# Performance work log

Hardware: AMD Instinct MI355X
Metric: run time of the kernel (lower is better)

## Reference

```python
import jax, jax.numpy as jnp
import numpy as np

N = 100000
E = 3200000
H_MLP = 30   # EdgeMLP hidden dim
H_GCN = 10   # GCNEvaluator hidden dim
D_IN = 6     # node_dim + token_dim


def setup_inputs() -> dict:
    key = jax.random.key(0)
    ks = jax.random.split(key, 24)
    s = 0.1
    inp = {
        "x": jax.random.normal(ks[0], (N, 1), jnp.float32),
        "token": jax.random.normal(ks[1], (N, 5), jnp.float32),
        "edge_attr_gen": jax.random.normal(ks[2], (E, 1), jnp.float32),
        "edge_attr_eval": jax.random.uniform(ks[3], (E, 2), jnp.float32),
        "gumbel": jax.random.gumbel(ks[4], (E, 2), jnp.float32),
        "edge_index": jax.random.randint(ks[5], (2, E), 0, N, jnp.int32),
        # EdgeMLP params: Linear(13,30), Linear(30,30), Linear(30,30), Linear(30,2)
        "W0": jax.random.normal(ks[6], (2 * D_IN + 1, H_MLP), jnp.float32) * s,
        "b0": jnp.zeros((H_MLP,), jnp.float32),
        "W1": jax.random.normal(ks[7], (H_MLP, H_MLP), jnp.float32) * s,
        "b1": jnp.zeros((H_MLP,), jnp.float32),
        "W2": jax.random.normal(ks[8], (H_MLP, H_MLP), jnp.float32) * s,
        "b2": jnp.zeros((H_MLP,), jnp.float32),
        "W3": jax.random.normal(ks[9], (H_MLP, 2), jnp.float32) * s,
        "b3": jnp.zeros((2,), jnp.float32),
        # GCNEvaluator params
        "Wl": jax.random.normal(ks[10], (1, 1), jnp.float32) * s,   # edge_weight_lin
        "bl": jnp.zeros((1,), jnp.float32),
        "Wc": jax.random.normal(ks[11], (D_IN, H_GCN), jnp.float32) * s,  # GCNConv weight
        "bc": jnp.zeros((H_GCN,), jnp.float32),
        "Wo": jax.random.normal(ks[12], (H_GCN, 1), jnp.float32) * s,     # output Linear
        "bo": jnp.zeros((1,), jnp.float32),
    }
    return inp


def reference(x, token, edge_attr_gen, edge_attr_eval, gumbel, edge_index,
              W0, b0, W1, b1, W2, b2, W3, b3, Wl, bl, Wc, bc, Wo, bo):
    src = edge_index[0]
    tgt = edge_index[1]
    x_all = jnp.concatenate([x, token], axis=-1)              # [N, 6]

    # ---- generate_graph: edge gather + concat + MLP ----
    ef = jnp.concatenate([x_all[src], x_all[tgt], edge_attr_gen], axis=-1)  # [E, 13]
    h = jax.nn.relu(ef @ W0 + b0)
    h = jax.nn.relu(h @ W1 + b1)
    h = jax.nn.relu(h @ W2 + b2)
    logits = h @ W3 + b3                                      # [E, 2]

    # gumbel_softmax(tau=1.0, hard=True) with straight-through
    y_soft = jax.nn.softmax(logits + gumbel, axis=-1)
    y_hard = jax.nn.one_hot(jnp.argmax(y_soft, axis=-1), 2, dtype=y_soft.dtype)
    y = y_hard + y_soft - jax.lax.stop_gradient(y_soft)
    edge_value = y[:, 1:2]                                    # [E, 1]

    # ---- evaluate_graph: GCNEvaluator ----
    combined = jnp.concatenate([edge_attr_eval, edge_value], axis=-1)  # [E, 3]
    mask = combined[:, -2] * (1.0 - combined[:, -1])
    ew = jax.nn.sigmoid((combined[:, :1] @ Wl + bl)[:, 0]) * mask      # [E]

    # GCNConv(add_self_loops=True, normalize=True)
    loop = jnp.arange(N, dtype=src.dtype)
    row = jnp.concatenate([src, loop])
    col = jnp.concatenate([tgt, loop])
    w = jnp.concatenate([ew, jnp.ones((N,), ew.dtype)])
    deg = jax.ops.segment_sum(w, col, num_segments=N)
    dis = jnp.where(deg > 0, jax.lax.rsqrt(jnp.where(deg > 0, deg, 1.0)), 0.0)
    norm = dis[row] * w * dis[col]
    xw = x_all @ Wc                                            # [N, 10]
    agg = jax.ops.segment_sum(norm[:, None] * xw[row], col, num_segments=N) + bc
    out = jax.nn.sigmoid(agg @ Wo + bo)                        # [N, 1]
    return out
```

## Files before the change

kernel.cpp:

```cpp
#include <hip/hip_runtime.h>

#define NN 100000
#define NE 3200000
#define HM 30
#define HG 10
#define MAXK 26
#define OVF_CAP 8192

typedef float __attribute__((ext_vector_type(2))) f32x2;

__device__ __forceinline__ f32x2 pkfma(f32x2 a, f32x2 b, f32x2 c) {
#if __has_builtin(__builtin_elementwise_fma)
    return __builtin_elementwise_fma(a, b, c);
#else
    f32x2 r; r.x = fmaf(a.x, b.x, c.x); r.y = fmaf(a.y, b.y, c.y); return r;
#endif
}

__global__ __launch_bounds__(256) void wtrans_kernel(
    const float* __restrict__ W0, const float* __restrict__ W1,
    const float* __restrict__ W2,
    float* __restrict__ W0T, float* __restrict__ W1T, float* __restrict__ W2T)
{
    for (int idx = threadIdx.x; idx < HM * 16; idx += 256) {
        int j = idx >> 4, i = idx & 15;
        W0T[idx] = (i < 13) ? W0[i * HM + j] : 0.f;
    }
    for (int idx = threadIdx.x; idx < HM * 32; idx += 256) {
        int j = idx >> 5, i = idx & 31;
        float v1 = (i < HM) ? W1[i * HM + j] : 0.f;
        float v2 = (i < HM) ? W2[i * HM + j] : 0.f;
        W1T[idx] = v1;
        W2T[idx] = v2;
    }
}

__global__ __launch_bounds__(256) void pack_kernel(
    const float* __restrict__ x, const float* __restrict__ token,
    const float* __restrict__ Wc,
    float* __restrict__ xall8, float* __restrict__ xwp)
{
    __shared__ float sWc[6 * HG];
    if (threadIdx.x < 6 * HG) sWc[threadIdx.x] = Wc[threadIdx.x];
    __syncthreads();

    int n = blockIdx.x * 256 + threadIdx.x;
    if (n >= NN) return;

    float xa[6];
    xa[0] = x[n];
    #pragma unroll
    for (int i = 0; i < 5; i++) xa[1 + i] = token[n * 5 + i];

    float4* x4 = (float4*)xall8;
    x4[n * 2 + 0] = make_float4(xa[0], xa[1], xa[2], xa[3]);
    x4[n * 2 + 1] = make_float4(xa[4], xa[5], 0.f, 0.f);

    float w[12];
    #pragma unroll
    for (int k = 0; k < HG; k++) {
        float a = 0.f;
        #pragma unroll
        for (int i = 0; i < 6; i++) a = fmaf(xa[i], sWc[i * HG + k], a);
        w[k] = a;
    }
    w[10] = 0.f; w[11] = 0.f;
    float4* wp = (float4*)(xwp + (size_t)n * 12);
    wp[0] = make_float4(w[0], w[1], w[2], w[3]);
    wp[1] = make_float4(w[4], w[5], w[6], w[7]);
    wp[2] = make_float4(w[8], w[9], w[10], w[11]);
}

__global__ __launch_bounds__(256, 2) void edge_mlp6_kernel(
    const float* __restrict__ xall8,
    const float* __restrict__ eg, const float* __restrict__ ee,
    const float* __restrict__ gum, const int* __restrict__ eidx,
    const float* __restrict__ W0T, const float* __restrict__ b0,
    const float* __restrict__ W1T, const float* __restrict__ b1,
    const float* __restrict__ W2T, const float* __restrict__ b2,
    const float* __restrict__ W3, const float* __restrict__ b3,
    const float* __restrict__ Wl, const float* __restrict__ bl,
    float2* __restrict__ slots, int* __restrict__ cnt, float* __restrict__ deg,
    int* __restrict__ ohead, int* __restrict__ onxt,
    float* __restrict__ ovf_w, int* __restrict__ ovf_s, int* __restrict__ novf)
{
    int e = blockIdx.x * 256 + threadIdx.x;
    int s = eidx[e];
    int t = eidx[NE + e];

    const float4* x4 = (const float4*)xall8;
    float4 qa = x4[s * 2], qb = x4[s * 2 + 1];
    float4 qc = x4[t * 2], qd = x4[t * 2 + 1];

    f32x2 ef2[7];
    ef2[0] = f32x2{ qa.x, qa.y };
    ef2[1] = f32x2{ qa.z, qa.w };
    ef2[2] = f32x2{ qb.x, qb.y };
    ef2[3] = f32x2{ qc.x, qc.y };
    ef2[4] = f32x2{ qc.z, qc.w };
    ef2[5] = f32x2{ qd.x, qd.y };
    ef2[6] = f32x2{ eg[e], 0.f };

    float h[HM], g[HM];

    #pragma unroll
    for (int j = 0; j < HM; j++) {
        const f32x2* w2 = (const f32x2*)(W0T + j * 16);
        f32x2 a2 = f32x2{ b0[j], 0.f };
        #pragma unroll
        for (int p = 0; p < 7; p++) a2 = pkfma(ef2[p], w2[p], a2);
        h[j] = fmaxf(a2.x + a2.y, 0.f);
    }

    {
        f32x2 hp[15];
        #pragma unroll
        for (int p = 0; p < 15; p++) hp[p] = f32x2{ h[2 * p], h[2 * p + 1] };
        #pragma unroll
        for (int j = 0; j < HM; j++) {
            const f32x2* w2 = (const f32x2*)(W1T + j * 32);
            f32x2 a2 = f32x2{ b1[j], 0.f };
            #pragma unroll
            for (int p = 0; p < 15; p++) a2 = pkfma(hp[p], w2[p], a2);
            g[j] = fmaxf(a2.x + a2.y, 0.f);
        }
    }
    {
        f32x2 gp[15];
        #pragma unroll
        for (int p = 0; p < 15; p++) gp[p] = f32x2{ g[2 * p], g[2 * p + 1] };
        #pragma unroll
        for (int j = 0; j < HM; j++) {
            const f32x2* w2 = (const f32x2*)(W2T + j * 32);
            f32x2 a2 = f32x2{ b2[j], 0.f };
            #pragma unroll
            for (int p = 0; p < 15; p++) a2 = pkfma(gp[p], w2[p], a2);
            h[j] = fmaxf(a2.x + a2.y, 0.f);
        }
    }

    float l0 = b3[0], l1 = b3[1];
    #pragma unroll
    for (int i = 0; i < HM; i++) {
        l0 = fmaf(h[i], W3[i * 2 + 0], l0);
        l1 = fmaf(h[i], W3[i * 2 + 1], l1);
    }

    const float2 g2 = ((const float2*)gum)[e];
    float v0 = l0 + g2.x;
    float v1 = l1 + g2.y;

    float ew = 0.f;
    if (!(v1 > v0)) {
        const float2 e2 = ((const float2*)ee)[e];
        float z = fmaf(e2.x, Wl[0], bl[0]);
        ew = e2.y / (1.f + __expf(-z));
    }
    if (ew != 0.f) {
        atomicAdd(&deg[t], ew);
        int slot = atomicAdd(&cnt[t], 1);
        if (slot < MAXK) {
            slots[(size_t)t * MAXK + slot] = make_float2(ew, __int_as_float(s));
        } else {
            int i = atomicAdd(novf, 1);
            if (i < OVF_CAP) {
                ovf_w[i] = ew;
                ovf_s[i] = s;
                onxt[i] = atomicExch(&ohead[t], i);
            }
        }
    }
}

__global__ __launch_bounds__(256) void node_dis_kernel(
    const float* __restrict__ deg, float* __restrict__ dis)
{
    int n = blockIdx.x * 256 + threadIdx.x;
    if (n >= NN) return;
    dis[n] = rsqrtf(deg[n] + 1.0f);
}

__global__ __launch_bounds__(256) void gather_out3_kernel(
    const float2* __restrict__ slots, const int* __restrict__ cnt,
    const int* __restrict__ ohead, const int* __restrict__ onxt,
    const float* __restrict__ ovf_w, const int* __restrict__ ovf_s,
    const float* __restrict__ xwp, const float* __restrict__ dis,
    const float* __restrict__ bc, const float* __restrict__ Wo,
    const float* __restrict__ bo, float* __restrict__ out)
{
    __shared__ float sbc[12], sWo[12], sbo;
    if (threadIdx.x < 12) {
        sbc[threadIdx.x] = (threadIdx.x < HG) ? bc[threadIdx.x] : 0.f;
        sWo[threadIdx.x] = (threadIdx.x < HG) ? Wo[threadIdx.x] : 0.f;
    }
    if (threadIdx.x == 0) sbo = bo[0];
    __syncthreads();

    int tg = blockIdx.x * 256 + threadIdx.x;
    int n = tg >> 2;
    int k = tg & 3;
    if (n >= NN) return;

    const float4* Z = (const float4*)xwp;
    float4 A0 = make_float4(0.f, 0.f, 0.f, 0.f), A1 = A0, A2 = A0;

    int c = cnt[n];
    int cc = c < MAXK ? c : MAXK;
    for (int j = k; j < cc; j += 4) {
        float2 p = slots[(size_t)n * MAXK + j];
        int s = __float_as_int(p.y);
        float w = p.x * dis[s];
        float4 z0 = Z[s * 3], z1 = Z[s * 3 + 1], z2 = Z[s * 3 + 2];
        A0.x = fmaf(w, z0.x, A0.x); A0.y = fmaf(w, z0.y, A0.y);
        A0.z = fmaf(w, z0.z, A0.z); A0.w = fmaf(w, z0.w, A0.w);
        A1.x = fmaf(w, z1.x, A1.x); A1.y = fmaf(w, z1.y, A1.y);
        A1.z = fmaf(w, z1.z, A1.z); A1.w = fmaf(w, z1.w, A1.w);
        A2.x = fmaf(w, z2.x, A2.x); A2.y = fmaf(w, z2.y, A2.y);
    }
    if (k == 0) {
        for (int i = ohead[n]; i >= 0; i = onxt[i]) {
            int s = ovf_s[i];
            float w = ovf_w[i] * dis[s];
            float4 z0 = Z[s * 3], z1 = Z[s * 3 + 1], z2 = Z[s * 3 + 2];
            A0.x = fmaf(w, z0.x, A0.x); A0.y = fmaf(w, z0.y, A0.y);
            A0.z = fmaf(w, z0.z, A0.z); A0.w = fmaf(w, z0.w, A0.w);
            A1.x = fmaf(w, z1.x, A1.x); A1.y = fmaf(w, z1.y, A1.y);
            A1.z = fmaf(w, z1.z, A1.z); A1.w = fmaf(w, z1.w, A1.w);
            A2.x = fmaf(w, z2.x, A2.x); A2.y = fmaf(w, z2.y, A2.y);
        }
        float wn = dis[n];
        float4 s0 = Z[n * 3], s1 = Z[n * 3 + 1], s2 = Z[n * 3 + 2];
        A0.x = fmaf(wn, s0.x, A0.x); A0.y = fmaf(wn, s0.y, A0.y);
        A0.z = fmaf(wn, s0.z, A0.z); A0.w = fmaf(wn, s0.w, A0.w);
        A1.x = fmaf(wn, s1.x, A1.x); A1.y = fmaf(wn, s1.y, A1.y);
        A1.z = fmaf(wn, s1.z, A1.z); A1.w = fmaf(wn, s1.w, A1.w);
        A2.x = fmaf(wn, s2.x, A2.x); A2.y = fmaf(wn, s2.y, A2.y);
    }

    float v[10] = { A0.x, A0.y, A0.z, A0.w, A1.x, A1.y, A1.z, A1.w, A2.x, A2.y };
    #pragma unroll
    for (int q = 0; q < 10; q++) {
        v[q] += __shfl_xor(v[q], 1);
        v[q] += __shfl_xor(v[q], 2);
    }

    if (k == 0) {
        float d = dis[n];
        float o = sbo;
        #pragma unroll
        for (int q = 0; q < HG; q++)
            o = fmaf(fmaf(v[q], d, sbc[q]), sWo[q], o);
        out[n] = 1.f / (1.f + __expf(-o));
    }
}

__global__ __launch_bounds__(256) void edge_mlp_kernel(
    const float* __restrict__ x, const float* __restrict__ token,
    const float* __restrict__ eg, const float* __restrict__ ee,
    const float* __restrict__ gum, const int* __restrict__ eidx,
    const float* __restrict__ W0, const float* __restrict__ b0,
    const float* __restrict__ W1, const float* __restrict__ b1,
    const float* __restrict__ W2, const float* __restrict__ b2,
    const float* __restrict__ W3, const float* __restrict__ b3,
    const float* __restrict__ Wl, const float* __restrict__ bl,
    float* __restrict__ ew_out, float* __restrict__ deg)
{
    __shared__ float sW0[13 * HM];
    __shared__ float sW1[HM * HM];
    __shared__ float sW2[HM * HM];
    __shared__ float sW3f[HM * 2];
    __shared__ float sb0[HM], sb1[HM], sb2[HM], sb3[2];
    __shared__ float sWl, sbl;

    for (int i = threadIdx.x; i < 13 * HM; i += 256) sW0[i] = W0[i];
    for (int i = threadIdx.x; i < HM * HM; i += 256) sW1[i] = W1[i];
    for (int i = threadIdx.x; i < HM * HM; i += 256) sW2[i] = W2[i];
    for (int i = threadIdx.x; i < HM * 2; i += 256) sW3f[i] = W3[i];
    if (threadIdx.x < HM) {
        sb0[threadIdx.x] = b0[threadIdx.x];
        sb1[threadIdx.x] = b1[threadIdx.x];
        sb2[threadIdx.x] = b2[threadIdx.x];
    }
    if (threadIdx.x < 2) sb3[threadIdx.x] = b3[threadIdx.x];
    if (threadIdx.x == 0) { sWl = Wl[0]; sbl = bl[0]; }
    __syncthreads();

    int e = blockIdx.x * 256 + threadIdx.x;
    if (e >= NE) return;
    int s = eidx[e];
    int t = eidx[NE + e];

    float ef[13];
    ef[0] = x[s];
    #pragma unroll
    for (int i = 0; i < 5; i++) ef[1 + i] = token[s * 5 + i];
    ef[6] = x[t];
    #pragma unroll
    for (int i = 0; i < 5; i++) ef[7 + i] = token[t * 5 + i];
    ef[12] = eg[e];

    float h[HM], h2[HM];
    #pragma unroll
    for (int j = 0; j < HM; j++) {
        float a = sb0[j];
        #pragma unroll
        for (int i = 0; i < 13; i++) a = fmaf(ef[i], sW0[i * HM + j], a);
        h[j] = a > 0.f ? a : 0.f;
    }
    #pragma unroll
    for (int j = 0; j < HM; j++) {
        float a = sb1[j];
        #pragma unroll
        for (int i = 0; i < HM; i++) a = fmaf(h[i], sW1[i * HM + j], a);
        h2[j] = a > 0.f ? a : 0.f;
    }
    #pragma unroll
    for (int j = 0; j < HM; j++) {
        float a = sb2[j];
        #pragma unroll
        for (int i = 0; i < HM; i++) a = fmaf(h2[i], sW2[i * HM + j], a);
        h[j] = a > 0.f ? a : 0.f;
    }
    float l0 = sb3[0], l1 = sb3[1];
    #pragma unroll
    for (int i = 0; i < HM; i++) {
        l0 = fmaf(h[i], sW3f[i * 2 + 0], l0);
        l1 = fmaf(h[i], sW3f[i * 2 + 1], l1);
    }
    const float2 g2 = ((const float2*)gum)[e];
    float v0 = l0 + g2.x, v1 = l1 + g2.y;
    float ew = 0.f;
    if (!(v1 > v0)) {
        const float2 ee2 = ((const float2*)ee)[e];
        float z = fmaf(ee2.x, sWl, sbl);
        ew = ee2.y / (1.f + __expf(-z));
    }
    ew_out[e] = ew;
    if (ew != 0.f) atomicAdd(&deg[t], ew);
}

__global__ __launch_bounds__(256) void node_pre_kernel(
    const float* __restrict__ x, const float* __restrict__ token,
    const float* __restrict__ Wc, const float* __restrict__ deg,
    float* __restrict__ xw, float* __restrict__ dis)
{
    __shared__ float sWc[6 * HG];
    if (threadIdx.x < 6 * HG) sWc[threadIdx.x] = Wc[threadIdx.x];
    __syncthreads();
    int n = blockIdx.x * 256 + threadIdx.x;
    if (n >= NN) return;
    float xa[6];
    xa[0] = x[n];
    #pragma unroll
    for (int i = 0; i < 5; i++) xa[1 + i] = token[n * 5 + i];
    #pragma unroll
    for (int k = 0; k < HG; k++) {
        float a = 0.f;
        #pragma unroll
        for (int i = 0; i < 6; i++) a = fmaf(xa[i], sWc[i * HG + k], a);
        xw[n * HG + k] = a;
    }
    dis[n] = rsqrtf(deg[n] + 1.0f);
}

__global__ __launch_bounds__(256) void edge_scatter_kernel(
    const int* __restrict__ eidx, const float* __restrict__ ew,
    const float* __restrict__ dis, const float* __restrict__ xw,
    float* __restrict__ agg)
{
    int e = blockIdx.x * 256 + threadIdx.x;
    if (e >= NE) return;
    float w = ew[e];
    if (w == 0.f) return;
    int s = eidx[e];
    int t = eidx[NE + e];
    float norm = dis[s] * w * dis[t];
    #pragma unroll
    for (int k = 0; k < HG; k++)
        atomicAdd(&agg[t * HG + k], norm * xw[s * HG + k]);
}

__global__ __launch_bounds__(256) void node_out_kernel(
    const float* __restrict__ agg, const float* __restrict__ xw,
    const float* __restrict__ dis, const float* __restrict__ bc,
    const float* __restrict__ Wo, const float* __restrict__ bo,
    float* __restrict__ out)
{
    __shared__ float sbc[HG], sWo[HG], sbo;
    if (threadIdx.x < HG) { sbc[threadIdx.x] = bc[threadIdx.x]; sWo[threadIdx.x] = Wo[threadIdx.x]; }
    if (threadIdx.x == 0) sbo = bo[0];
    __syncthreads();
    int n = blockIdx.x * 256 + threadIdx.x;
    if (n >= NN) return;
    float d = dis[n];
    float self = d * d;
    float acc = sbo;
    #pragma unroll
    for (int k = 0; k < HG; k++) {
        float v = agg[n * HG + k] + xw[n * HG + k] * self + sbc[k];
        acc = fmaf(v, sWo[k], acc);
    }
    out[n] = 1.f / (1.f + __expf(-acc));
}

extern "C" void kernel_launch(void* const* d_in, const int* in_sizes, int n_in,
                              void* d_out, int out_size, void* d_ws, size_t ws_size,
                              hipStream_t stream) {
    const float* x   = (const float*)d_in[0];
    const float* tok = (const float*)d_in[1];
    const float* eg  = (const float*)d_in[2];
    const float* ee  = (const float*)d_in[3];
    const float* gum = (const float*)d_in[4];
    const int*   ei  = (const int*)d_in[5];
    const float* W0  = (const float*)d_in[6];
    const float* b0  = (const float*)d_in[7];
    const float* W1  = (const float*)d_in[8];
    const float* b1  = (const float*)d_in[9];
    const float* W2  = (const float*)d_in[10];
    const float* b2  = (const float*)d_in[11];
    const float* W3  = (const float*)d_in[12];
    const float* b3  = (const float*)d_in[13];
    const float* Wl  = (const float*)d_in[14];
    const float* bl  = (const float*)d_in[15];
    const float* Wc  = (const float*)d_in[16];
    const float* bc  = (const float*)d_in[17];
    const float* Wo  = (const float*)d_in[18];
    const float* bo  = (const float*)d_in[19];
    float* out = (float*)d_out;

    dim3 blk(256);
    dim3 egrid(NE / 256);
    dim3 ngrid((NN + 255) / 256);
    dim3 g4grid((NN * 4 + 255) / 256);

    size_t off_xall8 = 0;
    size_t off_xwp   = off_xall8 + (size_t)NN * 8;
    size_t off_slots = off_xwp + (size_t)NN * 12;
    size_t off_cnt   = off_slots + (size_t)NN * MAXK * 2;
    size_t off_novf  = off_cnt + NN;
    size_t off_deg   = off_novf + 1;
    size_t off_dis   = off_deg + NN;
    size_t off_ohead = off_dis + NN;
    size_t off_ovfw  = off_ohead + NN;
    size_t off_ovfs  = off_ovfw + OVF_CAP;
    size_t off_onxt  = off_ovfs + OVF_CAP;
    size_t off_w0t   = (off_onxt + OVF_CAP + 15) & ~(size_t)15;
    size_t off_w1t   = off_w0t + 30 * 16;
    size_t off_w2t   = off_w1t + 30 * 32;
    size_t need_new  = (off_w2t + 30 * 32) * sizeof(float);

    if (ws_size >= need_new) {
        float*  ws    = (float*)d_ws;
        float*  xall8 = ws + off_xall8;
        float*  xwp   = ws + off_xwp;
        float2* slots = (float2*)(ws + off_slots);
        int*    cnt   = (int*)(ws + off_cnt);
        int*    novf  = (int*)(ws + off_novf);
        float*  deg   = ws + off_deg;
        float*  dis   = ws + off_dis;
        int*    ohead = (int*)(ws + off_ohead);
        float*  ovf_w = ws + off_ovfw;
        int*    ovf_s = (int*)(ws + off_ovfs);
        int*    onxt  = (int*)(ws + off_onxt);
        float*  W0T   = ws + off_w0t;
        float*  W1T   = ws + off_w1t;
        float*  W2T   = ws + off_w2t;

        hipMemsetAsync(cnt, 0, (size_t)(2 * NN + 1) * sizeof(int), stream);
        hipMemsetAsync(ohead, 0xFF, (size_t)NN * sizeof(int), stream);

        wtrans_kernel<<<dim3(1), blk, 0, stream>>>(W0, W1, W2, W0T, W1T, W2T);
        pack_kernel<<<ngrid, blk, 0, stream>>>(x, tok, Wc, xall8, xwp);
        edge_mlp6_kernel<<<egrid, blk, 0, stream>>>(xall8, eg, ee, gum, ei,
                                                    W0T, b0, W1T, b1, W2T, b2,
                                                    W3, b3, Wl, bl, slots, cnt, deg,
                                                    ohead, onxt, ovf_w, ovf_s, novf);
        node_dis_kernel<<<ngrid, blk, 0, stream>>>(deg, dis);
        gather_out3_kernel<<<g4grid, blk, 0, stream>>>(slots, cnt, ohead, onxt,
                                                       ovf_w, ovf_s, xwp, dis,
                                                       bc, Wo, bo, out);
    } else {
        float* ws  = (float*)d_ws;
        float* ew  = ws;
        float* deg = ew + NE;
        float* agg = deg + NN;
        float* xw  = agg + (size_t)NN * HG;
        float* dis = xw + (size_t)NN * HG;

        hipMemsetAsync(deg, 0, (size_t)(NN + (size_t)NN * HG) * sizeof(float), stream);
        edge_mlp_kernel<<<egrid, blk, 0, stream>>>(x, tok, eg, ee, gum, ei,
                                                   W0, b0, W1, b1, W2, b2, W3, b3,
                                                   Wl, bl, ew, deg);
        node_pre_kernel<<<ngrid, blk, 0, stream>>>(x, tok, Wc, deg, xw, dis);
        edge_scatter_kernel<<<egrid, blk, 0, stream>>>(ei, ew, dis, xw, agg);
        node_out_kernel<<<ngrid, blk, 0, stream>>>(agg, xw, dis, bc, Wo, bo, out);
    }
}
```

Before: 396.8 us.

## Compute degree from slot lists and prescale node features by dis

```diff
diff --git a/kernel.cpp b/kernel.cpp
--- a/kernel.cpp
+++ b/kernel.cpp
@@ -71,7 +71,7 @@
     wp[2] = make_float4(w[8], w[9], w[10], w[11]);
 }
 
-__global__ __launch_bounds__(256, 2) void edge_mlp6_kernel(
+__global__ __launch_bounds__(256, 2) void edge_mlp7_kernel(
     const float* __restrict__ xall8,
     const float* __restrict__ eg, const float* __restrict__ ee,
     const float* __restrict__ gum, const int* __restrict__ eidx,
@@ -80,7 +80,7 @@
     const float* __restrict__ W2T, const float* __restrict__ b2,
     const float* __restrict__ W3, const float* __restrict__ b3,
     const float* __restrict__ Wl, const float* __restrict__ bl,
-    float2* __restrict__ slots, int* __restrict__ cnt, float* __restrict__ deg,
+    float2* __restrict__ slots, int* __restrict__ cnt,
     int* __restrict__ ohead, int* __restrict__ onxt,
     float* __restrict__ ovf_w, int* __restrict__ ovf_s, int* __restrict__ novf)
 {
@@ -157,7 +157,6 @@
         ew = e2.y / (1.f + __expf(-z));
     }
     if (ew != 0.f) {
-        atomicAdd(&deg[t], ew);
         int slot = atomicAdd(&cnt[t], 1);
         if (slot < MAXK) {
             slots[(size_t)t * MAXK + slot] = make_float2(ew, __int_as_float(s));
@@ -172,19 +171,38 @@
     }
 }
 
-__global__ __launch_bounds__(256) void node_dis_kernel(
-    const float* __restrict__ deg, float* __restrict__ dis)
+__global__ __launch_bounds__(256) void node_deg_kernel(
+    const float2* __restrict__ slots, const int* __restrict__ cnt,
+    const int* __restrict__ ohead, const int* __restrict__ onxt,
+    const float* __restrict__ ovf_w,
+    float* __restrict__ xwp, float* __restrict__ dis)
 {
     int n = blockIdx.x * 256 + threadIdx.x;
     if (n >= NN) return;
-    dis[n] = rsqrtf(deg[n] + 1.0f);
-}
-
-__global__ __launch_bounds__(256) void gather_out3_kernel(
+
+    int c = cnt[n];
+    int cc = c < MAXK ? c : MAXK;
+    float deg = 0.f;
+    for (int j = 0; j < cc; j++) deg += slots[(size_t)n * MAXK + j].x;
+    for (int i = ohead[n]; i >= 0; i = onxt[i]) deg += ovf_w[i];
+
+    float d = rsqrtf(deg + 1.0f);
+    dis[n] = d;
+
+    float4* wp = (float4*)(xwp + (size_t)n * 12);
+    #pragma unroll
+    for (int q = 0; q < 3; q++) {
+        float4 v = wp[q];
+        v.x *= d; v.y *= d; v.z *= d; v.w *= d;
+        wp[q] = v;
+    }
+}
+
+__global__ __launch_bounds__(256) void gather_out4_kernel(
     const float2* __restrict__ slots, const int* __restrict__ cnt,
     const int* __restrict__ ohead, const int* __restrict__ onxt,
     const float* __restrict__ ovf_w, const int* __restrict__ ovf_s,
-    const float* __restrict__ xwp, const float* __restrict__ dis,
+    const float* __restrict__ z, const float* __restrict__ dis,
     const float* __restrict__ bc, const float* __restrict__ Wo,
     const float* __restrict__ bo, float* __restrict__ out)
 {
@@ -201,15 +219,15 @@
     int k = tg & 3;
     if (n >= NN) return;
 
-    const float4* Z = (const float4*)xwp;
+    const float4* Z = (const float4*)z;
     float4 A0 = make_float4(0.f, 0.f, 0.f, 0.f), A1 = A0, A2 = A0;
 
     int c = cnt[n];
     int cc = c < MAXK ? c : MAXK;
     for (int j = k; j < cc; j += 4) {
         float2 p = slots[(size_t)n * MAXK + j];
+        float w = p.x;
         int s = __float_as_int(p.y);
-        float w = p.x * dis[s];
         float4 z0 = Z[s * 3], z1 = Z[s * 3 + 1], z2 = Z[s * 3 + 2];
         A0.x = fmaf(w, z0.x, A0.x); A0.y = fmaf(w, z0.y, A0.y);
         A0.z = fmaf(w, z0.z, A0.z); A0.w = fmaf(w, z0.w, A0.w);
@@ -219,8 +237,8 @@
     }
     if (k == 0) {
         for (int i = ohead[n]; i >= 0; i = onxt[i]) {
+            float w = ovf_w[i];
             int s = ovf_s[i];
-            float w = ovf_w[i] * dis[s];
             float4 z0 = Z[s * 3], z1 = Z[s * 3 + 1], z2 = Z[s * 3 + 2];
             A0.x = fmaf(w, z0.x, A0.x); A0.y = fmaf(w, z0.y, A0.y);
             A0.z = fmaf(w, z0.z, A0.z); A0.w = fmaf(w, z0.w, A0.w);
@@ -228,13 +246,10 @@
             A1.z = fmaf(w, z1.z, A1.z); A1.w = fmaf(w, z1.w, A1.w);
             A2.x = fmaf(w, z2.x, A2.x); A2.y = fmaf(w, z2.y, A2.y);
         }
-        float wn = dis[n];
         float4 s0 = Z[n * 3], s1 = Z[n * 3 + 1], s2 = Z[n * 3 + 2];
-        A0.x = fmaf(wn, s0.x, A0.x); A0.y = fmaf(wn, s0.y, A0.y);
-        A0.z = fmaf(wn, s0.z, A0.z); A0.w = fmaf(wn, s0.w, A0.w);
-        A1.x = fmaf(wn, s1.x, A1.x); A1.y = fmaf(wn, s1.y, A1.y);
-        A1.z = fmaf(wn, s1.z, A1.z); A1.w = fmaf(wn, s1.w, A1.w);
-        A2.x = fmaf(wn, s2.x, A2.x); A2.y = fmaf(wn, s2.y, A2.y);
+        A0.x += s0.x; A0.y += s0.y; A0.z += s0.z; A0.w += s0.w;
+        A1.x += s1.x; A1.y += s1.y; A1.z += s1.z; A1.w += s1.w;
+        A2.x += s2.x; A2.y += s2.y;
     }
 
     float v[10] = { A0.x, A0.y, A0.z, A0.w, A1.x, A1.y, A1.z, A1.w, A2.x, A2.y };
@@ -438,8 +453,7 @@
     size_t off_slots = off_xwp + (size_t)NN * 12;
     size_t off_cnt   = off_slots + (size_t)NN * MAXK * 2;
     size_t off_novf  = off_cnt + NN;
-    size_t off_deg   = off_novf + 1;
-    size_t off_dis   = off_deg + NN;
+    size_t off_dis   = off_novf + 1;
     size_t off_ohead = off_dis + NN;
     size_t off_ovfw  = off_ohead + NN;
     size_t off_ovfs  = off_ovfw + OVF_CAP;
@@ -456,7 +470,6 @@
         float2* slots = (float2*)(ws + off_slots);
         int*    cnt   = (int*)(ws + off_cnt);
         int*    novf  = (int*)(ws + off_novf);
-        float*  deg   = ws + off_deg;
         float*  dis   = ws + off_dis;
         int*    ohead = (int*)(ws + off_ohead);
         float*  ovf_w = ws + off_ovfw;
@@ -466,17 +479,18 @@
         float*  W1T   = ws + off_w1t;
         float*  W2T   = ws + off_w2t;
 
-        hipMemsetAsync(cnt, 0, (size_t)(2 * NN + 1) * sizeof(int), stream);
+        hipMemsetAsync(cnt, 0, (size_t)(NN + 1) * sizeof(int), stream);
         hipMemsetAsync(ohead, 0xFF, (size_t)NN * sizeof(int), stream);
 
         wtrans_kernel<<<dim3(1), blk, 0, stream>>>(W0, W1, W2, W0T, W1T, W2T);
         pack_kernel<<<ngrid, blk, 0, stream>>>(x, tok, Wc, xall8, xwp);
-        edge_mlp6_kernel<<<egrid, blk, 0, stream>>>(xall8, eg, ee, gum, ei,
+        edge_mlp7_kernel<<<egrid, blk, 0, stream>>>(xall8, eg, ee, gum, ei,
                                                     W0T, b0, W1T, b1, W2T, b2,
-                                                    W3, b3, Wl, bl, slots, cnt, deg,
+                                                    W3, b3, Wl, bl, slots, cnt,
                                                     ohead, onxt, ovf_w, ovf_s, novf);
-        node_dis_kernel<<<ngrid, blk, 0, stream>>>(deg, dis);
-        gather_out3_kernel<<<g4grid, blk, 0, stream>>>(slots, cnt, ohead, onxt,
+        node_deg_kernel<<<ngrid, blk, 0, stream>>>(slots, cnt, ohead, onxt, ovf_w,
+                                                   xwp, dis);
+        gather_out4_kernel<<<g4grid, blk, 0, stream>>>(slots, cnt, ohead, onxt,
                                                        ovf_w, ovf_s, xwp, dis,
                                                        bc, Wo, bo, out);
     } else {
```

Result: faster. 375.7 us (-5.3%).
